# Kernel tuning notes

Hardware: AMD Instinct MI355X
Metric: run time of the kernel (lower is better)

## Reference

```python
import jax, jax.numpy as jnp
from jax import lax
import numpy as np

B, N, H, K = 64, 256, 1024, 3  # batch, num_proposals, hidden_dim, conv kernel size
LN_EPS = 1e-5


def setup_inputs() -> dict:
    key = jax.random.key(0)
    k1, k2, k3 = jax.random.split(key, 3)
    scale = 1.0 / np.sqrt(H)
    return {
        "f": jax.random.normal(k1, (B, N, H), dtype=jnp.float32),
        "k": jax.random.normal(k2, (B, N, H), dtype=jnp.float32),
        "W_lin": jax.random.normal(k3, (N * K, H), dtype=jnp.float32) * scale,
        "b_lin": jnp.zeros((N * K,), dtype=jnp.float32),
        "ln_gamma": jnp.ones((H,), dtype=jnp.float32),
        "ln_beta": jnp.zeros((H,), dtype=jnp.float32),
    }


def _conv_one(x, w):
    # x: [N, H] (channels, length); w: [N_out, N_in, K]
    # PyTorch F.conv1d is cross-correlation, same as lax conv with no flip.
    y = lax.conv_general_dilated(
        x[None], w, window_strides=(1,), padding="SAME",
        dimension_numbers=("NCH", "OIH", "NCH"))
    return y[0]  # [N, H]


def reference(f, k, W_lin, b_lin, ln_gamma, ln_beta):
    # Dynamic weight generation: [B, N, H] -> [B, N, N*K] -> [B, N, N, K]
    weight = jnp.einsum("bnh,oh->bno", f, W_lin) + b_lin
    weight = weight.reshape(B, N, N, K)
    # Per-sample dynamic conv1d over the hidden dim (batched via vmap)
    out = jax.vmap(_conv_one)(k, weight)  # [B, N, H]
    # LayerNorm over hidden dim
    mu = jnp.mean(out, axis=-1, keepdims=True)
    var = jnp.var(out, axis=-1, keepdims=True)
    out = (out - mu) * lax.rsqrt(var + LN_EPS) * ln_gamma + ln_beta
    return out
```

## Files before the change

kernel.cpp:

```cpp
#include <hip/hip_runtime.h>
#include <math.h>

#define Bsz 64
#define Nn  256
#define Hh  1024
#define NK  768

typedef __bf16 bf16;
typedef bf16 bf16x4 __attribute__((ext_vector_type(4)));
typedef bf16 bf16x8 __attribute__((ext_vector_type(8)));
typedef float floatx4 __attribute__((ext_vector_type(4)));

__device__ __forceinline__ void gl_lds16(const bf16* g, bf16* l) {
    __builtin_amdgcn_global_load_lds(
        (__attribute__((address_space(1))) void*)(g),
        (__attribute__((address_space(3))) void*)(l), 16, 0, 0);
}

__global__ __launch_bounds__(256) void cast_bf16_kernel(
    const float* __restrict__ src, bf16* __restrict__ dst, int n4)
{
    int i = blockIdx.x * 256 + threadIdx.x;
    if (i < n4) {
        float4 v = ((const float4*)src)[i];
        bf16x4 o = { (bf16)v.x, (bf16)v.y, (bf16)v.z, (bf16)v.w };
        ((bf16x4*)dst)[i] = o;
    }
}

__global__ __launch_bounds__(256) void gemm1_mfma(
    const bf16* __restrict__ A,
    const bf16* __restrict__ Bw,
    const float* __restrict__ bias,
    bf16* __restrict__ wgt3)
{
    __shared__ bf16 As[128 * 32];
    __shared__ bf16 Bs[128 * 32];
    const int tid  = threadIdx.x;
    const int wave = tid >> 6, lane = tid & 63;
    const int row0 = blockIdx.y * 128;
    const int col0 = blockIdx.x * 128;

    const int s0 = (wave * 2 + 0) * 64 + lane;
    const int s1 = (wave * 2 + 1) * 64 + lane;
    const bf16* gA0 = A  + (size_t)(row0 + (s0 >> 2)) * Hh + (s0 & 3) * 8;
    const bf16* gA1 = A  + (size_t)(row0 + (s1 >> 2)) * Hh + (s1 & 3) * 8;
    const bf16* gB0 = Bw + (size_t)(col0 + (s0 >> 2)) * Hh + (s0 & 3) * 8;
    const bf16* gB1 = Bw + (size_t)(col0 + (s1 >> 2)) * Hh + (s1 & 3) * 8;
    bf16* lA0 = &As[(wave * 2 + 0) * 512];
    bf16* lA1 = &As[(wave * 2 + 1) * 512];
    bf16* lB0 = &Bs[(wave * 2 + 0) * 512];
    bf16* lB1 = &Bs[(wave * 2 + 1) * 512];

    const int wm = wave & 1, wn = wave >> 1;
    const int fm = lane & 15, koct = (lane >> 4) * 8;

    floatx4 zero = {0.f, 0.f, 0.f, 0.f};
    floatx4 acc[4][4];
    #pragma unroll
    for (int i = 0; i < 4; ++i)
        #pragma unroll
        for (int j = 0; j < 4; ++j) acc[i][j] = zero;

    for (int k0 = 0; k0 < Hh; k0 += 32) {
        gl_lds16(gA0 + k0, lA0);
        gl_lds16(gA1 + k0, lA1);
        gl_lds16(gB0 + k0, lB0);
        gl_lds16(gB1 + k0, lB1);
        __syncthreads();
        bf16x8 af[4], bfr[4];
        #pragma unroll
        for (int mt = 0; mt < 4; ++mt)
            af[mt] = *(const bf16x8*)&As[(wm * 64 + mt * 16 + fm) * 32 + koct];
        #pragma unroll
        for (int nt = 0; nt < 4; ++nt)
            bfr[nt] = *(const bf16x8*)&Bs[(wn * 64 + nt * 16 + fm) * 32 + koct];
        #pragma unroll
        for (int mt = 0; mt < 4; ++mt)
            #pragma unroll
            for (int nt = 0; nt < 4; ++nt)
                acc[mt][nt] = __builtin_amdgcn_mfma_f32_16x16x32_bf16(
                    af[mt], bfr[nt], acc[mt][nt], 0, 0, 0);
        __syncthreads();
    }

    const int b = row0 >> 8;
    #pragma unroll
    for (int nt = 0; nt < 4; ++nt) {
        int col = col0 + wn * 64 + nt * 16 + fm;
        float bl = bias[col];
        int ii = col / 3;
        int tt = col - ii * 3;
        bf16* dst = wgt3 + ((size_t)(b * 3 + tt) << 16) + ii;
        #pragma unroll
        for (int mt = 0; mt < 4; ++mt) {
            int nr = (row0 & 255) + wm * 64 + mt * 16 + (lane >> 4) * 4;
            #pragma unroll
            for (int r = 0; r < 4; ++r)
                dst[(size_t)(nr + r) << 8] = (bf16)(acc[mt][nt][r] + bl);
        }
    }
}

__global__ __launch_bounds__(256) void conv_mfma(
    const bf16* __restrict__ kbf,
    const bf16* __restrict__ wgt3,
    bf16* __restrict__ conv)
{
    __shared__ bf16 As[3 * 128 * 32];
    __shared__ bf16 Ks[130 * 40];
    const int tid  = threadIdx.x;
    const int wave = tid >> 6, lane = tid & 63;
    const int b  = blockIdx.z;
    const int o0 = blockIdx.y * 128;
    const int h0 = blockIdx.x * 128;
    const int wm = wave & 1, wn = wave >> 1;
    const int fm = lane & 15, koct = (lane >> 4) * 8;

    const bf16* gA[6];
    bf16* lA[6];
    #pragma unroll
    for (int j = 0; j < 6; ++j) {
        int s = (wave * 6 + j) * 64 + lane;
        int t = s >> 9, rem = s & 511;
        int o = rem >> 2, iq = rem & 3;
        gA[j] = wgt3 + ((size_t)(b * 3 + t) << 16) + ((size_t)(o0 + o) << 8) + iq * 8;
        lA[j] = &As[(wave * 6 + j) * 512];
    }
    const int ki  = tid & 31;
    const int kho = tid >> 5;
    const bf16* kbase = kbf + ((size_t)b << 18);

    floatx4 zero = {0.f, 0.f, 0.f, 0.f};
    floatx4 acc[4][4];
    #pragma unroll
    for (int i = 0; i < 4; ++i)
        #pragma unroll
        for (int j = 0; j < 4; ++j) acc[i][j] = zero;

    for (int ic = 0; ic < 8; ++ic) {
        const int i0 = ic * 32;
        __syncthreads();
        #pragma unroll
        for (int j = 0; j < 6; ++j) gl_lds16(gA[j] + i0, lA[j]);
        #pragma unroll
        for (int p = 0; p < 2; ++p) {
            int ho = kho + p * 8;
            bf16x8 v = *(const bf16x8*)&kbase[(size_t)(i0 + ki) * Hh + h0 + ho * 8];
            #pragma unroll
            for (int j = 0; j < 8; ++j)
                Ks[(1 + ho * 8 + j) * 40 + ki] = v[j];
        }
        if (tid < 32) {
            Ks[tid] = (h0 > 0) ? kbase[(size_t)(i0 + tid) * Hh + h0 - 1] : (bf16)0.f;
        } else if (tid < 64) {
            int i2 = tid - 32;
            Ks[129 * 40 + i2] = (h0 + 128 < Hh)
                ? kbase[(size_t)(i0 + i2) * Hh + h0 + 128] : (bf16)0.f;
        }
        __syncthreads();
        #pragma unroll
        for (int t = 0; t < 3; ++t) {
            bf16x8 af[4], bfr[4];
            #pragma unroll
            for (int mt = 0; mt < 4; ++mt)
                af[mt] = *(const bf16x8*)&As[t * 4096 + (wm * 64 + mt * 16 + fm) * 32 + koct];
            #pragma unroll
            for (int nt = 0; nt < 4; ++nt)
                bfr[nt] = *(const bf16x8*)&Ks[(wn * 64 + nt * 16 + fm + t) * 40 + koct];
            #pragma unroll
            for (int mt = 0; mt < 4; ++mt)
                #pragma unroll
                for (int nt = 0; nt < 4; ++nt)
                    acc[mt][nt] = __builtin_amdgcn_mfma_f32_16x16x32_bf16(
                        af[mt], bfr[nt], acc[mt][nt], 0, 0, 0);
        }
    }

    #pragma unroll
    for (int mt = 0; mt < 4; ++mt) {
        int o = o0 + wm * 64 + mt * 16 + (lane >> 4) * 4;
        #pragma unroll
        for (int nt = 0; nt < 4; ++nt) {
            int h = h0 + wn * 64 + nt * 16 + fm;
            #pragma unroll
            for (int r = 0; r < 4; ++r)
                conv[((size_t)(b * 256 + o + r) << 10) + h] = (bf16)acc[mt][nt][r];
        }
    }
}

__global__ __launch_bounds__(256) void ln_kernel(
    const bf16* __restrict__ conv, const float* __restrict__ gamma,
    const float* __restrict__ beta, float* __restrict__ out)
{
    const int row = blockIdx.x;
    const int tid = threadIdx.x;
    bf16x4 v = ((const bf16x4*)(conv + ((size_t)row << 10)))[tid];
    float x[4] = {(float)v[0], (float)v[1], (float)v[2], (float)v[3]};
    float s1 = x[0] + x[1] + x[2] + x[3];
    float s2 = x[0]*x[0] + x[1]*x[1] + x[2]*x[2] + x[3]*x[3];
    #pragma unroll
    for (int m = 1; m < 64; m <<= 1) {
        s1 += __shfl_xor(s1, m, 64);
        s2 += __shfl_xor(s2, m, 64);
    }
    __shared__ float r1[4], r2[4];
    if ((tid & 63) == 0) { r1[tid >> 6] = s1; r2[tid >> 6] = s2; }
    __syncthreads();
    float S1 = r1[0] + r1[1] + r1[2] + r1[3];
    float S2 = r2[0] + r2[1] + r2[2] + r2[3];
    float mu   = S1 * (1.0f / 1024.0f);
    float var  = S2 * (1.0f / 1024.0f) - mu * mu;
    float rstd = rsqrtf(var + 1e-5f);
    float4 g  = ((const float4*)gamma)[tid];
    float4 be = ((const float4*)beta)[tid];
    float4 o;
    o.x = (x[0] - mu) * rstd * g.x + be.x;
    o.y = (x[1] - mu) * rstd * g.y + be.y;
    o.z = (x[2] - mu) * rstd * g.z + be.z;
    o.w = (x[3] - mu) * rstd * g.w + be.w;
    ((float4*)(out + ((size_t)row << 10)))[tid] = o;
}

extern "C" void kernel_launch(void* const* d_in, const int* in_sizes, int n_in,
                              void* d_out, int out_size, void* d_ws, size_t ws_size,
                              hipStream_t stream) {
    const float* f     = (const float*)d_in[0];
    const float* kin   = (const float*)d_in[1];
    const float* W_lin = (const float*)d_in[2];
    const float* b_lin = (const float*)d_in[3];
    const float* gamma = (const float*)d_in[4];
    const float* beta  = (const float*)d_in[5];
    float* out = (float*)d_out;

    char* ws = (char*)d_ws;
    bf16* fbf  = (bf16*)(ws);
    bf16* kbf  = (bf16*)(ws + 33554432);
    bf16* wlbf = (bf16*)(ws + 67108864);
    bf16* wgt3 = (bf16*)(ws + 68681728);
    bf16* conv = fbf;

    cast_bf16_kernel<<<16384, 256, 0, stream>>>(f,   fbf,  4194304);
    cast_bf16_kernel<<<16384, 256, 0, stream>>>(kin, kbf,  4194304);
    cast_bf16_kernel<<<768,   256, 0, stream>>>(W_lin, wlbf, 196608);

    gemm1_mfma<<<dim3(6, 128), 256, 0, stream>>>(fbf, wlbf, b_lin, wgt3);
    conv_mfma<<<dim3(8, 2, 64), 256, 0, stream>>>(kbf, wgt3, conv);
    ln_kernel<<<16384, 256, 0, stream>>>(conv, gamma, beta, out);
}
```

Before: 317.5 us.

## Fuse k cast into conv, merge casts, double-depth gemm1 K-step, widen conv tile

The separate cast of k to bf16 is dropped: the conv kernel now reads fp32 k directly and converts while staging into LDS. The f and W_lin casts are merged into one launch, and gemm1 loads 64 K-elements per barrier pair instead of 32. The conv tile is widened to 256 columns with 8 N-subtiles per wave, and its result is written as fp32 straight into the output buffer, which LayerNorm then normalizes in place. This removes one full read/write pass over k and some launches, in exchange for heavier fp32 reads in conv, doubled accumulator registers, and a larger fp32 intermediate.

After: 287.3 us. 1.11x faster.

```diff
diff --git a/kernel.cpp b/kernel.cpp
--- a/kernel.cpp
+++ b/kernel.cpp
@@ -17,14 +17,22 @@
         (__attribute__((address_space(3))) void*)(l), 16, 0, 0);
 }
 
-__global__ __launch_bounds__(256) void cast_bf16_kernel(
-    const float* __restrict__ src, bf16* __restrict__ dst, int n4)
+__global__ __launch_bounds__(256) void cast2_kernel(
+    const float* __restrict__ f, const float* __restrict__ wl,
+    bf16* __restrict__ fbf, bf16* __restrict__ wlbf)
 {
     int i = blockIdx.x * 256 + threadIdx.x;
-    if (i < n4) {
-        float4 v = ((const float4*)src)[i];
+    if (i < 4194304) {
+        float4 v = ((const float4*)f)[i];
         bf16x4 o = { (bf16)v.x, (bf16)v.y, (bf16)v.z, (bf16)v.w };
-        ((bf16x4*)dst)[i] = o;
+        ((bf16x4*)fbf)[i] = o;
+    } else {
+        int j = i - 4194304;
+        if (j < 196608) {
+            float4 v = ((const float4*)wl)[j];
+            bf16x4 o = { (bf16)v.x, (bf16)v.y, (bf16)v.z, (bf16)v.w };
+            ((bf16x4*)wlbf)[j] = o;
+        }
     }
 }
 
@@ -34,23 +42,27 @@
     const float* __restrict__ bias,
     bf16* __restrict__ wgt3)
 {
-    __shared__ bf16 As[128 * 32];
-    __shared__ bf16 Bs[128 * 32];
+    __shared__ bf16 As[2][128 * 32];
+    __shared__ bf16 Bs[2][128 * 32];
     const int tid  = threadIdx.x;
     const int wave = tid >> 6, lane = tid & 63;
     const int row0 = blockIdx.y * 128;
     const int col0 = blockIdx.x * 128;
 
-    const int s0 = (wave * 2 + 0) * 64 + lane;
-    const int s1 = (wave * 2 + 1) * 64 + lane;
-    const bf16* gA0 = A  + (size_t)(row0 + (s0 >> 2)) * Hh + (s0 & 3) * 8;
-    const bf16* gA1 = A  + (size_t)(row0 + (s1 >> 2)) * Hh + (s1 & 3) * 8;
-    const bf16* gB0 = Bw + (size_t)(col0 + (s0 >> 2)) * Hh + (s0 & 3) * 8;
-    const bf16* gB1 = Bw + (size_t)(col0 + (s1 >> 2)) * Hh + (s1 & 3) * 8;
-    bf16* lA0 = &As[(wave * 2 + 0) * 512];
-    bf16* lA1 = &As[(wave * 2 + 1) * 512];
-    bf16* lB0 = &Bs[(wave * 2 + 0) * 512];
-    bf16* lB1 = &Bs[(wave * 2 + 1) * 512];
+    const bf16* gA[4]; const bf16* gB[4];
+    bf16* lA[4]; bf16* lB[4];
+    #pragma unroll
+    for (int j = 0; j < 4; ++j) {
+        int sg  = wave * 4 + j;
+        int reg = sg >> 3;
+        int wi  = sg & 7;
+        int row = wi * 16 + (lane >> 2);
+        int quad = lane & 3;
+        gA[j] = A  + (size_t)(row0 + row) * Hh + reg * 32 + quad * 8;
+        gB[j] = Bw + (size_t)(col0 + row) * Hh + reg * 32 + quad * 8;
+        lA[j] = &As[reg][wi * 512];
+        lB[j] = &Bs[reg][wi * 512];
+    }
 
     const int wm = wave & 1, wn = wave >> 1;
     const int fm = lane & 15, koct = (lane >> 4) * 8;
@@ -62,25 +74,29 @@
         #pragma unroll
         for (int j = 0; j < 4; ++j) acc[i][j] = zero;
 
-    for (int k0 = 0; k0 < Hh; k0 += 32) {
-        gl_lds16(gA0 + k0, lA0);
-        gl_lds16(gA1 + k0, lA1);
-        gl_lds16(gB0 + k0, lB0);
-        gl_lds16(gB1 + k0, lB1);
-        __syncthreads();
-        bf16x8 af[4], bfr[4];
-        #pragma unroll
-        for (int mt = 0; mt < 4; ++mt)
-            af[mt] = *(const bf16x8*)&As[(wm * 64 + mt * 16 + fm) * 32 + koct];
-        #pragma unroll
-        for (int nt = 0; nt < 4; ++nt)
-            bfr[nt] = *(const bf16x8*)&Bs[(wn * 64 + nt * 16 + fm) * 32 + koct];
-        #pragma unroll
-        for (int mt = 0; mt < 4; ++mt)
+    for (int k0 = 0; k0 < Hh; k0 += 64) {
+        #pragma unroll
+        for (int j = 0; j < 4; ++j) {
+            gl_lds16(gA[j] + k0, lA[j]);
+            gl_lds16(gB[j] + k0, lB[j]);
+        }
+        __syncthreads();
+        #pragma unroll
+        for (int q = 0; q < 2; ++q) {
+            bf16x8 af[4], bfr[4];
+            #pragma unroll
+            for (int mt = 0; mt < 4; ++mt)
+                af[mt] = *(const bf16x8*)&As[q][(wm * 64 + mt * 16 + fm) * 32 + koct];
             #pragma unroll
             for (int nt = 0; nt < 4; ++nt)
-                acc[mt][nt] = __builtin_amdgcn_mfma_f32_16x16x32_bf16(
-                    af[mt], bfr[nt], acc[mt][nt], 0, 0, 0);
+                bfr[nt] = *(const bf16x8*)&Bs[q][(wn * 64 + nt * 16 + fm) * 32 + koct];
+            #pragma unroll
+            for (int mt = 0; mt < 4; ++mt)
+                #pragma unroll
+                for (int nt = 0; nt < 4; ++nt)
+                    acc[mt][nt] = __builtin_amdgcn_mfma_f32_16x16x32_bf16(
+                        af[mt], bfr[nt], acc[mt][nt], 0, 0, 0);
+        }
         __syncthreads();
     }
 
@@ -102,18 +118,18 @@
     }
 }
 
-__global__ __launch_bounds__(256) void conv_mfma(
-    const bf16* __restrict__ kbf,
+__global__ __launch_bounds__(256, 2) void conv_mfma(
+    const float* __restrict__ kin,
     const bf16* __restrict__ wgt3,
-    bf16* __restrict__ conv)
+    float* __restrict__ out)
 {
     __shared__ bf16 As[3 * 128 * 32];
-    __shared__ bf16 Ks[130 * 40];
+    __shared__ bf16 Ks[258 * 40];
     const int tid  = threadIdx.x;
     const int wave = tid >> 6, lane = tid & 63;
     const int b  = blockIdx.z;
     const int o0 = blockIdx.y * 128;
-    const int h0 = blockIdx.x * 128;
+    const int h0 = blockIdx.x * 256;
     const int wm = wave & 1, wn = wave >> 1;
     const int fm = lane & 15, koct = (lane >> 4) * 8;
 
@@ -129,14 +145,14 @@
     }
     const int ki  = tid & 31;
     const int kho = tid >> 5;
-    const bf16* kbase = kbf + ((size_t)b << 18);
+    const float* kb = kin + (size_t)b * Nn * Hh;
 
     floatx4 zero = {0.f, 0.f, 0.f, 0.f};
-    floatx4 acc[4][4];
+    floatx4 acc[4][8];
     #pragma unroll
     for (int i = 0; i < 4; ++i)
         #pragma unroll
-        for (int j = 0; j < 4; ++j) acc[i][j] = zero;
+        for (int j = 0; j < 8; ++j) acc[i][j] = zero;
 
     for (int ic = 0; ic < 8; ++ic) {
         const int i0 = ic * 32;
@@ -144,34 +160,38 @@
         #pragma unroll
         for (int j = 0; j < 6; ++j) gl_lds16(gA[j] + i0, lA[j]);
         #pragma unroll
-        for (int p = 0; p < 2; ++p) {
+        for (int p = 0; p < 4; ++p) {
             int ho = kho + p * 8;
-            bf16x8 v = *(const bf16x8*)&kbase[(size_t)(i0 + ki) * Hh + h0 + ho * 8];
-            #pragma unroll
-            for (int j = 0; j < 8; ++j)
-                Ks[(1 + ho * 8 + j) * 40 + ki] = v[j];
+            const float* src = kb + (size_t)(i0 + ki) * Hh + h0 + ho * 8;
+            float4 v0 = ((const float4*)src)[0];
+            float4 v1 = ((const float4*)src)[1];
+            int rb = (1 + ho * 8) * 40 + ki;
+            Ks[rb + 0 * 40] = (bf16)v0.x; Ks[rb + 1 * 40] = (bf16)v0.y;
+            Ks[rb + 2 * 40] = (bf16)v0.z; Ks[rb + 3 * 40] = (bf16)v0.w;
+            Ks[rb + 4 * 40] = (bf16)v1.x; Ks[rb + 5 * 40] = (bf16)v1.y;
+            Ks[rb + 6 * 40] = (bf16)v1.z; Ks[rb + 7 * 40] = (bf16)v1.w;
         }
         if (tid < 32) {
-            Ks[tid] = (h0 > 0) ? kbase[(size_t)(i0 + tid) * Hh + h0 - 1] : (bf16)0.f;
+            Ks[tid] = (h0 > 0) ? (bf16)kb[(size_t)(i0 + tid) * Hh + h0 - 1] : (bf16)0.f;
         } else if (tid < 64) {
             int i2 = tid - 32;
-            Ks[129 * 40 + i2] = (h0 + 128 < Hh)
-                ? kbase[(size_t)(i0 + i2) * Hh + h0 + 128] : (bf16)0.f;
+            Ks[257 * 40 + i2] = (h0 + 256 < Hh)
+                ? (bf16)kb[(size_t)(i0 + i2) * Hh + h0 + 256] : (bf16)0.f;
         }
         __syncthreads();
         #pragma unroll
         for (int t = 0; t < 3; ++t) {
-            bf16x8 af[4], bfr[4];
+            bf16x8 af[4], bfr[8];
             #pragma unroll
             for (int mt = 0; mt < 4; ++mt)
                 af[mt] = *(const bf16x8*)&As[t * 4096 + (wm * 64 + mt * 16 + fm) * 32 + koct];
             #pragma unroll
-            for (int nt = 0; nt < 4; ++nt)
-                bfr[nt] = *(const bf16x8*)&Ks[(wn * 64 + nt * 16 + fm + t) * 40 + koct];
+            for (int nt = 0; nt < 8; ++nt)
+                bfr[nt] = *(const bf16x8*)&Ks[(wn * 128 + nt * 16 + fm + t) * 40 + koct];
             #pragma unroll
             for (int mt = 0; mt < 4; ++mt)
                 #pragma unroll
-                for (int nt = 0; nt < 4; ++nt)
+                for (int nt = 0; nt < 8; ++nt)
                     acc[mt][nt] = __builtin_amdgcn_mfma_f32_16x16x32_bf16(
                         af[mt], bfr[nt], acc[mt][nt], 0, 0, 0);
         }
@@ -181,23 +201,24 @@
     for (int mt = 0; mt < 4; ++mt) {
         int o = o0 + wm * 64 + mt * 16 + (lane >> 4) * 4;
         #pragma unroll
-        for (int nt = 0; nt < 4; ++nt) {
-            int h = h0 + wn * 64 + nt * 16 + fm;
+        for (int nt = 0; nt < 8; ++nt) {
+            int h = h0 + wn * 128 + nt * 16 + fm;
             #pragma unroll
             for (int r = 0; r < 4; ++r)
-                conv[((size_t)(b * 256 + o + r) << 10) + h] = (bf16)acc[mt][nt][r];
+                out[((size_t)(b * 256 + o + r) << 10) + h] = acc[mt][nt][r];
         }
     }
 }
 
 __global__ __launch_bounds__(256) void ln_kernel(
-    const bf16* __restrict__ conv, const float* __restrict__ gamma,
-    const float* __restrict__ beta, float* __restrict__ out)
+    float* __restrict__ io, const float* __restrict__ gamma,
+    const float* __restrict__ beta)
 {
     const int row = blockIdx.x;
     const int tid = threadIdx.x;
-    bf16x4 v = ((const bf16x4*)(conv + ((size_t)row << 10)))[tid];
-    float x[4] = {(float)v[0], (float)v[1], (float)v[2], (float)v[3]};
+    float* p = io + ((size_t)row << 10);
+    float4 v = ((const float4*)p)[tid];
+    float x[4] = {v.x, v.y, v.z, v.w};
     float s1 = x[0] + x[1] + x[2] + x[3];
     float s2 = x[0]*x[0] + x[1]*x[1] + x[2]*x[2] + x[3]*x[3];
     #pragma unroll
@@ -220,7 +241,7 @@
     o.y = (x[1] - mu) * rstd * g.y + be.y;
     o.z = (x[2] - mu) * rstd * g.z + be.z;
     o.w = (x[3] - mu) * rstd * g.w + be.w;
-    ((float4*)(out + ((size_t)row << 10)))[tid] = o;
+    ((float4*)p)[tid] = o;
 }
 
 extern "C" void kernel_launch(void* const* d_in, const int* in_sizes, int n_in,
@@ -236,16 +257,11 @@
 
     char* ws = (char*)d_ws;
     bf16* fbf  = (bf16*)(ws);
-    bf16* kbf  = (bf16*)(ws + 33554432);
-    bf16* wlbf = (bf16*)(ws + 67108864);
-    bf16* wgt3 = (bf16*)(ws + 68681728);
-    bf16* conv = fbf;
-
-    cast_bf16_kernel<<<16384, 256, 0, stream>>>(f,   fbf,  4194304);
-    cast_bf16_kernel<<<16384, 256, 0, stream>>>(kin, kbf,  4194304);
-    cast_bf16_kernel<<<768,   256, 0, stream>>>(W_lin, wlbf, 196608);
-
+    bf16* wlbf = (bf16*)(ws + 33554432);
+    bf16* wgt3 = (bf16*)(ws + 35127296);
+
+    cast2_kernel<<<17152, 256, 0, stream>>>(f, W_lin, fbf, wlbf);
     gemm1_mfma<<<dim3(6, 128), 256, 0, stream>>>(fbf, wlbf, b_lin, wgt3);
-    conv_mfma<<<dim3(8, 2, 64), 256, 0, stream>>>(kbf, wgt3, conv);
-    ln_kernel<<<16384, 256, 0, stream>>>(conv, gamma, beta, out);
-}
+    conv_mfma<<<dim3(4, 2, 64), 256, 0, stream>>>(kin, wgt3, out);
+    ln_kernel<<<16384, 256, 0, stream>>>(out, gamma, beta);
+}
```
